# Kernel optimization log

Measured on AMD Instinct MI355X. Metric: run time of the kernel, lower is better.

Reference implementation:

```python
import jax, jax.numpy as jnp
import numpy as np
import math

NUM_LEAD = 12
PATCHES = 100  # patch_num_v * patch_num_h = 5 * 20
HEADS = 12
HID = 768
DH = HID // HEADS  # 64
SEQ = NUM_LEAD * PATCHES + NUM_LEAD + 1  # 1213
INTER = 3072
BATCH = 8


def _layer_norm(x, g, b, eps=1e-12):
    u = x.mean(-1, keepdims=True)
    s = ((x - u) ** 2).mean(-1, keepdims=True)
    return g * (x - u) / jnp.sqrt(s + eps) + b


def _lead_mask():
    # make_mask with fusion == 0: additive bias applied to query rows [0, NUM_LEAD+1)
    cols = jnp.arange(SEQ)
    # CLS row: 1 at lead-token positions 1..NUM_LEAD
    cls_row = jnp.where((cols >= 1) & (cols < NUM_LEAD + 1), 1.0, 0.0)
    # Lead rows: 1 everywhere except own patch block
    i = jnp.arange(NUM_LEAD)[:, None]
    start = NUM_LEAD + 1 + PATCHES * i
    in_block = (cols[None, :] >= start) & (cols[None, :] < start + PATCHES)
    lead_rows = jnp.where(in_block, 0.0, 1.0)
    mask = jnp.concatenate([cls_row[None, :], lead_rows], axis=0)  # [NUM_LEAD+1, SEQ]
    return mask * (-99999.0)


def setup_inputs() -> dict:
    key = jax.random.key(0)
    ks = jax.random.split(key, 12)
    std = 0.02
    d = {
        "hidden_states": jax.random.normal(ks[0], (BATCH, SEQ, HID), jnp.float32),
        "attention_mask": jnp.zeros((BATCH, 1, 1, SEQ), jnp.float32),
        "Wq": jax.random.normal(ks[1], (HID, HID), jnp.float32) * std,
        "bq": jnp.zeros((HID,), jnp.float32),
        "Wk": jax.random.normal(ks[2], (HID, HID), jnp.float32) * std,
        "bk": jnp.zeros((HID,), jnp.float32),
        "Wv": jax.random.normal(ks[3], (HID, HID), jnp.float32) * std,
        "bv": jnp.zeros((HID,), jnp.float32),
        "Wo": jax.random.normal(ks[4], (HID, HID), jnp.float32) * std,
        "bo": jnp.zeros((HID,), jnp.float32),
        "gamma1": jnp.ones((HID,), jnp.float32),
        "beta1": jnp.zeros((HID,), jnp.float32),
        "Wi": jax.random.normal(ks[5], (HID, INTER), jnp.float32) * std,
        "bi": jnp.zeros((INTER,), jnp.float32),
        "Wd": jax.random.normal(ks[6], (INTER, HID), jnp.float32) * std,
        "bd": jnp.zeros((HID,), jnp.float32),
        "gamma2": jnp.ones((HID,), jnp.float32),
        "beta2": jnp.zeros((HID,), jnp.float32),
    }
    return d


def reference(hidden_states, attention_mask, Wq, bq, Wk, bk, Wv, bv, Wo, bo,
              gamma1, beta1, Wi, bi, Wd, bd, gamma2, beta2):
    B, S, _ = hidden_states.shape

    def heads(x):  # [B,S,HID] -> [B,H,S,DH]
        return x.reshape(B, S, HEADS, DH).transpose(0, 2, 1, 3)

    q = heads(hidden_states @ Wq + bq)
    k = heads(hidden_states @ Wk + bk)
    v = heads(hidden_states @ Wv + bv)

    scores = jnp.einsum("bhqd,bhkd->bhqk", q, k) / math.sqrt(DH)
    scores = scores + attention_mask  # broadcast [B,1,1,S]
    lead_mask = _lead_mask()  # [NUM_LEAD+1, SEQ]
    scores = scores.at[:, :, : NUM_LEAD + 1, :].add(lead_mask[None, None])

    probs = jax.nn.softmax(scores, axis=-1)  # dropout is identity in eval
    ctx = jnp.einsum("bhqk,bhkd->bhqd", probs, v)
    ctx = ctx.transpose(0, 2, 1, 3).reshape(B, S, HID)

    attn_out = _layer_norm(ctx @ Wo + bo + hidden_states, gamma1, beta1)
    inter = jax.nn.gelu(attn_out @ Wi + bi, approximate=False)  # exact erf gelu
    out = _layer_norm(inter @ Wd + bd + attn_out, gamma2, beta2)
    return out
```

## Files before the change

kernel.cpp:

```cpp
#include <hip/hip_runtime.h>
#include <hip/hip_bf16.h>
#include <stdint.h>

typedef unsigned short u16;
typedef unsigned int u32;
typedef __attribute__((ext_vector_type(8))) short frag8;
typedef __attribute__((ext_vector_type(4))) float f32x4;

#define SEQ 1213
#define BATCH 8
#define HEADS 12
#define DH 64
#define HID 768
#define INTER 3072
#define BS (BATCH*SEQ)
#define LOG2E 1.44269504088896f

#define MFMA(a,b,c) __builtin_amdgcn_mfma_f32_16x16x32_bf16(a,b,c,0,0,0)

__device__ __forceinline__ float b2f(u16 u){ u32 i=((u32)u)<<16; float f; __builtin_memcpy(&f,&i,4); return f; }
__device__ __forceinline__ u16 f2b(float f){ u32 i; __builtin_memcpy(&i,&f,4); i = i + 0x7fffu + ((i>>16)&1u); return (u16)(i>>16); }
__device__ __forceinline__ u32 pack2(float a, float b){ return (u32)f2b(a) | ((u32)f2b(b)<<16); }

__device__ __forceinline__ void async16(const u16* g, u16* l){
  __builtin_amdgcn_global_load_lds((const __attribute__((address_space(1))) u32*)(uintptr_t)g,
                                   (__attribute__((address_space(3))) u32*)(uintptr_t)l, 16, 0, 0);
}

__global__ __launch_bounds__(256) void convert_arr(const void* __restrict__ src,
  u16* __restrict__ dst, int n8, const u16* __restrict__ probe)
{
  const bool f32 = (probe[0] == 0);
  int i = blockIdx.x*256 + threadIdx.x;
  if (i >= n8) return;
  u16 tmp[8];
  if (f32){
    const float* s = (const float*)src + (size_t)i*8;
#pragma unroll
    for (int j=0;j<8;j++) tmp[j] = f2b(s[j]);
  } else {
    *(uint4*)tmp = *((const uint4*)src + i);
  }
  *((uint4*)dst + i) = *(const uint4*)tmp;
}

__global__ __launch_bounds__(256) void convert_small(
  const void* bq, const void* bk, const void* bv, const void* bo,
  const void* bi, const void* bd, const void* g1, const void* be1,
  const void* g2, const void* be2, const void* am,
  u16* __restrict__ dst, const u16* __restrict__ probe)
{
  const int starts[12] = {0,768,1536,2304,3072,6144,6912,7680,8448,9216,9984,19688};
  const void* srcs[11] = {bq,bk,bv,bo,bi,bd,g1,be1,g2,be2,am};
  const bool f32 = (probe[0] == 0);
  int e = (blockIdx.x*256 + threadIdx.x) * 8;
  if (e >= 19688) return;
  int seg = 0;
#pragma unroll
  for (int k=1;k<11;k++) if (starts[k] <= e) seg = k;
  int off = e - starts[seg];
  const void* s = srcs[seg];
  u16 tmp[8];
  if (f32){
    const float* sf = (const float*)s + off;
#pragma unroll
    for (int j=0;j<8;j++) tmp[j] = f2b(sf[j]);
  } else {
    const u16* sh = (const u16*)s + off;
#pragma unroll
    for (int j=0;j<8;j++) tmp[j] = sh[j];
  }
  *(uint4*)(dst + e) = *(const uint4*)tmp;
}

__global__ __launch_bounds__(256) void transpose2(const void* __restrict__ in,
  u16* __restrict__ out, int R, int C, const u16* __restrict__ probe)
{
  const bool f32 = (probe[0] == 0);
  __shared__ u16 tile[32][33];
  const int bx = blockIdx.x*32, by = blockIdx.y*32;
  const int tx = threadIdx.x & 31, ty = threadIdx.x >> 5;
  if (f32){
    const float* inf_ = (const float*)in;
#pragma unroll
    for (int i=ty;i<32;i+=8) tile[i][tx] = f2b(inf_[(size_t)(by+i)*C + bx+tx]);
  } else {
    const u16* inh = (const u16*)in;
#pragma unroll
    for (int i=ty;i<32;i+=8) tile[i][tx] = inh[(size_t)(by+i)*C + bx+tx];
  }
  __syncthreads();
#pragma unroll
  for (int i=ty;i<32;i+=8) out[(size_t)(bx+i)*R + by+tx] = tile[tx][i];
}

__device__ __forceinline__ void gemm_tile(
    const u16* __restrict__ A, const u16* __restrict__ BT,
    int M, int K, int m0, int n0,
    u16* ldsA, u16* ldsB, f32x4 acc[4][4])
{
  const int t = threadIdx.x;
  const int w = t >> 6, l = t & 63;
  const int lw = l & 15, lh = l >> 4;
  const int rowo = (w >> 1) << 6;
  const int colo = (w & 1) << 6;
  const int srow = w*8 + (l>>3);
  const int scol = ((l&7) ^ ((l>>3)&7)) * 8;

  const u16* gpA[4]; const u16* gpB[4];
  u16* lpA[4]; u16* lpB[4];
#pragma unroll
  for (int p=0;p<4;p++){
    int ra = m0 + p*32 + srow; if (ra >= M) ra = M-1;
    gpA[p] = A  + (size_t)ra*K + scol;
    gpB[p] = BT + (size_t)(n0 + p*32 + srow)*K + scol;
    lpA[p] = ldsA + (p*32 + w*8)*64 + l*8;
    lpB[p] = ldsB + (p*32 + w*8)*64 + l*8;
  }

  const int slot0 = lw & 7;
  for (int k0 = 0; k0 < K; k0 += 64) {
    __syncthreads();
#pragma unroll
    for (int p=0;p<4;p++) async16(gpA[p] + k0, lpA[p]);
#pragma unroll
    for (int p=0;p<4;p++) async16(gpB[p] + k0, lpB[p]);
    __syncthreads();
#pragma unroll
    for (int kk=0;kk<2;kk++){
      const int slot = ((kk*4 + lh) ^ slot0) * 8;
      frag8 af[4], bf[4];
#pragma unroll
      for (int mi=0;mi<4;mi++) af[mi] = *(const frag8*)(ldsA + (rowo + mi*16 + lw)*64 + slot);
#pragma unroll
      for (int ni=0;ni<4;ni++) bf[ni] = *(const frag8*)(ldsB + (colo + ni*16 + lw)*64 + slot);
#pragma unroll
      for (int mi=0;mi<4;mi++)
#pragma unroll
        for (int ni=0;ni<4;ni++)
          acc[mi][ni] = MFMA(af[mi], bf[ni], acc[mi][ni]);
    }
  }
}

__global__ __launch_bounds__(256,2) void gemm_qkv(
  const u16* __restrict__ A, const u16* __restrict__ BT,
  const u16* __restrict__ bq, const u16* __restrict__ bk, const u16* __restrict__ bv,
  u16* __restrict__ Qo, u16* __restrict__ Ko, u16* __restrict__ Vo)
{
  __shared__ __align__(16) u16 ldsA[128*64];
  __shared__ __align__(16) u16 ldsB[128*64];
  f32x4 acc[4][4];
#pragma unroll
  for (int i=0;i<4;i++)
#pragma unroll
    for (int j=0;j<4;j++) acc[i][j] = 0.f;
  const int m0 = blockIdx.x*128, n0 = blockIdx.y*128;
  gemm_tile(A, BT, BS, HID, m0, n0, ldsA, ldsB, acc);
  const int t=threadIdx.x, w=t>>6, l=t&63, lw=l&15, lh=l>>4;
  const int rowb = m0 + ((w>>1)<<6), colb = n0 + ((w&1)<<6);
#pragma unroll
  for (int ni=0;ni<4;ni++){
    int cc = colb + ni*16 + lw;
    int which = cc / HID;
    int n2 = cc - which*HID;
    int h = n2 >> 6, d = n2 & 63;
    const u16* bp = which==0 ? bq : (which==1 ? bk : bv);
    u16* op = which==0 ? Qo : (which==1 ? Ko : Vo);
    float bias = b2f(bp[n2]);
    float scale = which==0 ? 0.125f : 1.0f;
#pragma unroll
    for (int mi=0;mi<4;mi++){
#pragma unroll
      for (int r=0;r<4;r++){
        int rr = rowb + mi*16 + lh*4 + r;
        if (rr < BS){
          int bi_ = rr / SEQ;
          int si  = rr - bi_*SEQ;
          float v = (acc[mi][ni][r] + bias) * scale;
          op[(((size_t)(bi_*HEADS + h))*SEQ + si)*64 + d] = f2b(v);
        }
      }
    }
  }
}

__global__ __launch_bounds__(256,2) void gemm_resid(
  const u16* __restrict__ A, const u16* __restrict__ BT,
  const u16* __restrict__ bias, const u16* __restrict__ resid,
  u16* __restrict__ out, int N, int K)
{
  __shared__ __align__(16) u16 ldsA[128*64];
  __shared__ __align__(16) u16 ldsB[128*64];
  f32x4 acc[4][4];
#pragma unroll
  for (int i=0;i<4;i++)
#pragma unroll
    for (int j=0;j<4;j++) acc[i][j] = 0.f;
  const int m0 = blockIdx.x*128, n0 = blockIdx.y*128;
  gemm_tile(A, BT, BS, K, m0, n0, ldsA, ldsB, acc);
  const int t=threadIdx.x, w=t>>6, l=t&63, lw=l&15, lh=l>>4;
  const int rowb = m0 + ((w>>1)<<6), colb = n0 + ((w&1)<<6);
#pragma unroll
  for (int ni=0;ni<4;ni++){
    int cc = colb + ni*16 + lw;
    float bv_ = b2f(bias[cc]);
#pragma unroll
    for (int mi=0;mi<4;mi++){
#pragma unroll
      for (int r=0;r<4;r++){
        int rr = rowb + mi*16 + lh*4 + r;
        if (rr < BS){
          float v = acc[mi][ni][r] + bv_ + b2f(resid[(size_t)rr*N + cc]);
          out[(size_t)rr*N + cc] = f2b(v);
        }
      }
    }
  }
}

__global__ __launch_bounds__(256,2) void gemm_gelu(
  const u16* __restrict__ A, const u16* __restrict__ BT,
  const u16* __restrict__ bias, u16* __restrict__ out, int N, int K)
{
  __shared__ __align__(16) u16 ldsA[128*64];
  __shared__ __align__(16) u16 ldsB[128*64];
  f32x4 acc[4][4];
#pragma unroll
  for (int i=0;i<4;i++)
#pragma unroll
    for (int j=0;j<4;j++) acc[i][j] = 0.f;
  const int m0 = blockIdx.x*128, n0 = blockIdx.y*128;
  gemm_tile(A, BT, BS, K, m0, n0, ldsA, ldsB, acc);
  const int t=threadIdx.x, w=t>>6, l=t&63, lw=l&15, lh=l>>4;
  const int rowb = m0 + ((w>>1)<<6), colb = n0 + ((w&1)<<6);
#pragma unroll
  for (int ni=0;ni<4;ni++){
    int cc = colb + ni*16 + lw;
    float bv_ = b2f(bias[cc]);
#pragma unroll
    for (int mi=0;mi<4;mi++){
#pragma unroll
      for (int r=0;r<4;r++){
        int rr = rowb + mi*16 + lh*4 + r;
        if (rr < BS){
          float v = acc[mi][ni][r] + bv_;
          v = 0.5f * v * (1.0f + erff(v * 0.70710678118654752f));
          out[(size_t)rr*N + cc] = f2b(v);
        }
      }
    }
  }
}

__global__ __launch_bounds__(512,1) void attn_kernel(
  const u16* __restrict__ Qb, const u16* __restrict__ Kb, const u16* __restrict__ Vb,
  const u16* __restrict__ amask, u16* __restrict__ ctx)
{
  __shared__ __align__(16) u16 sQP[128*72];
  __shared__ __align__(16) u16 sK[64*72];
  __shared__ __align__(16) u16 sV[64*72];
  __shared__ float sEm[64];
  const int t = threadIdx.x, w = t>>6, l = t&63, lw = l&15, lh = l>>4;
  const int bh = blockIdx.y, b = bh / HEADS;
  const int q0 = blockIdx.x * 128;
  const int h = bh % HEADS;
  const size_t hb = (size_t)bh * SEQ * 64;
  const u16* Qp = Qb + hb;
  const u16* Kp = Kb + hb;
  const u16* Vp = Vb + hb;

  {
    int r = t >> 3, c = t & 7;
#pragma unroll
    for (int i=0;i<2;i++){
      int rr = i*64 + r;
      int s = q0 + rr; if (s > SEQ-1) s = SEQ-1;
      *(uint4*)(sQP + rr*72 + c*8) = *(const uint4*)(Qp + (size_t)s*64 + c*8);
    }
  }
  __syncthreads();
  frag8 qa[2];
#pragma unroll
  for (int kk=0;kk<2;kk++) qa[kk] = *(const frag8*)(sQP + (w*16 + lw)*72 + kk*32 + lh*8);
  u16* pw = sQP + w*16*72;

  float l_p = 0.f;
  f32x4 o[4];
#pragma unroll
  for (int i=0;i<4;i++) o[i] = 0.f;
  const bool leadwave = (q0 == 0) && (w == 0);

  const int rr = t >> 3, c = t & 7;
  const int scol = (((rr>>3) ^ (c&3))<<3) + (rr&7);

  uint4 kreg, vreg; float emreg = 0.f;
  {
    int s = rr; if (s > SEQ-1) s = SEQ-1;
    kreg = *(const uint4*)(Kp + (size_t)s*64 + c*8);
    vreg = *(const uint4*)(Vp + (size_t)s*64 + c*8);
    if (t < 64) emreg = b2f(amask[b*SEQ + t]) * LOG2E;
  }

  const int nkt = (SEQ + 63) / 64;
  for (int kt = 0; kt < nkt; kt++) {
    __syncthreads();
    {
      *(uint4*)(sK + rr*72 + c*8) = kreg;
      const u16* vp = (const u16*)&vreg;
#pragma unroll
      for (int j=0;j<8;j++)
        sV[(c*8 + j)*72 + scol] = vp[j];
      if (t < 64) sEm[t] = emreg;
    }
    __syncthreads();
    if (kt+1 < nkt){
      int s = (kt+1)*64 + rr; if (s > SEQ-1) s = SEQ-1;
      kreg = *(const uint4*)(Kp + (size_t)s*64 + c*8);
      vreg = *(const uint4*)(Vp + (size_t)s*64 + c*8);
      if (t < 64){
        int sg = (kt+1)*64 + t;
        emreg = (sg < SEQ) ? b2f(amask[b*SEQ + sg]) * LOG2E : -1e30f;
      }
    }

    f32x4 st[4];
#pragma unroll
    for (int si=0;si<4;si++){
      f32x4 a0 = 0.f;
#pragma unroll
      for (int kk=0;kk<2;kk++){
        frag8 kf = *(const frag8*)(sK + (si*16 + lw)*72 + kk*32 + lh*8);
        a0 = MFMA(kf, qa[kk], a0);
      }
      st[si] = a0;
    }

#pragma unroll
    for (int si=0;si<4;si++){
      f32x4 emv = *(const f32x4*)(sEm + si*16 + lh*4);
#pragma unroll
      for (int r=0;r<4;r++)
        st[si][r] = exp2f(fmaf(st[si][r], LOG2E, emv[r]));
    }
    if (leadwave){
#pragma unroll
      for (int si=0;si<4;si++){
#pragma unroll
        for (int r=0;r<4;r++){
          int sg = kt*64 + si*16 + lh*4 + r;
          int q = lw;
          float p = st[si][r];
          if (q == 0){
            if (sg >= 1 && sg < 13) p = 0.f;
          } else if (q < 13){
            int stt = 13 + 100*(q-1);
            if (!(sg >= stt && sg < stt+100)) p = 0.f;
          }
          st[si][r] = p;
        }
      }
    }
#pragma unroll
    for (int si=0;si<4;si++)
#pragma unroll
      for (int r=0;r<4;r++) l_p += st[si][r];

#pragma unroll
    for (int si=0;si<4;si++){
      *(u32*)(pw + lw*72 + si*16 + lh*4)     = pack2(st[si][0], st[si][1]);
      *(u32*)(pw + lw*72 + si*16 + lh*4 + 2) = pack2(st[si][2], st[si][3]);
    }
    __threadfence_block();

#pragma unroll
    for (int kk=0;kk<2;kk++){
      frag8 pf = *(const frag8*)(pw + lw*72 + kk*32 + lh*8);
#pragma unroll
      for (int ni=0;ni<4;ni++){
        int d = ni*16 + lw;
        int grp = (kk*4 + lh) ^ ((d>>3) & 3);
        frag8 vf = *(const frag8*)(sV + d*72 + (grp<<3));
        o[ni] = MFMA(pf, vf, o[ni]);
      }
    }
  }

  l_p += __shfl_xor(l_p, 16);
  l_p += __shfl_xor(l_p, 32);

#pragma unroll
  for (int r=0;r<4;r++){
    float lf = __shfl(l_p, (l & 48) + ((l >> 4) << 2) + r);
    int qg = q0 + w*16 + lh*4 + r;
    if (qg < SEQ){
      float inv = 1.0f / lf;
#pragma unroll
      for (int ni=0;ni<4;ni++){
        ctx[((size_t)(b*SEQ) + qg)*HID + h*64 + ni*16 + lw] = f2b(o[ni][r] * inv);
      }
    }
  }
}

__global__ __launch_bounds__(256) void ln_kernel(const u16* __restrict__ y,
  const u16* __restrict__ g, const u16* __restrict__ be,
  u16* __restrict__ outb, float* __restrict__ outf)
{
  const int row = blockIdx.x, t = threadIdx.x;
  const u16* yp = y + (size_t)row*HID;
  float x0 = b2f(yp[t]), x1 = b2f(yp[t+256]), x2 = b2f(yp[t+512]);
  float s = x0 + x1 + x2;
  __shared__ float red[4];
#pragma unroll
  for (int off=1; off<64; off<<=1) s += __shfl_xor(s, off);
  if ((t & 63) == 0) red[t>>6] = s;
  __syncthreads();
  float u = (red[0]+red[1]+red[2]+red[3]) * (1.0f/768.0f);
  float d0=x0-u, d1=x1-u, d2=x2-u;
  float s2 = d0*d0 + d1*d1 + d2*d2;
  __syncthreads();
#pragma unroll
  for (int off=1; off<64; off<<=1) s2 += __shfl_xor(s2, off);
  if ((t & 63) == 0) red[t>>6] = s2;
  __syncthreads();
  float var = (red[0]+red[1]+red[2]+red[3]) * (1.0f/768.0f);
  float rstd = rsqrtf(var + 1e-12f);
  float v0 = b2f(g[t])    *(d0*rstd) + b2f(be[t]);
  float v1 = b2f(g[t+256])*(d1*rstd) + b2f(be[t+256]);
  float v2 = b2f(g[t+512])*(d2*rstd) + b2f(be[t+512]);
  if (outf){
    float* op = outf + (size_t)row*HID;
    op[t] = v0; op[t+256] = v1; op[t+512] = v2;
  } else {
    u16* op = outb + (size_t)row*HID;
    op[t] = f2b(v0); op[t+256] = f2b(v1); op[t+512] = f2b(v2);
  }
}

extern "C" void kernel_launch(void* const* d_in, const int* in_sizes, int n_in,
                              void* d_out, int out_size, void* d_ws, size_t ws_size,
                              hipStream_t stream)
{
  const void* hidden = d_in[0];
  const void* amask  = d_in[1];
  const void* Wq = d_in[2];  const void* bq = d_in[3];
  const void* Wk = d_in[4];  const void* bk = d_in[5];
  const void* Wv = d_in[6];  const void* bv = d_in[7];
  const void* Wo = d_in[8];  const void* bo = d_in[9];
  const void* g1 = d_in[10]; const void* be1= d_in[11];
  const void* Wi = d_in[12]; const void* bi = d_in[13];
  const void* Wd = d_in[14]; const void* bd = d_in[15];
  const void* g2 = d_in[16]; const void* be2= d_in[17];
  const u16* probe = (const u16*)g1;

  char* ws = (char*)d_ws;
  size_t off = 0;
  auto alloc = [&](size_t elems)->u16* {
    u16* p = (u16*)(ws + off);
    off += ((elems*2 + 255) & ~(size_t)255);
    return p;
  };
  u16* hiddenC = alloc((size_t)BS*HID);
  u16* smallC  = alloc((size_t)19688);
  u16* WqkvT = alloc((size_t)2304*768);
  u16* WoT   = alloc((size_t)768*768);
  u16* WiT   = alloc((size_t)3072*768);
  u16* WdT   = alloc((size_t)768*3072);
  u16* Qb    = alloc((size_t)BS*HID);
  u16* Kb    = alloc((size_t)BS*HID);
  u16* Vb    = alloc((size_t)BS*HID);
  u16* y1    = alloc((size_t)BS*HID);
  u16* interb = Qb;
  u16* ctxb  = alloc((size_t)BS*HID);
  u16* attn_out = alloc((size_t)BS*HID);
  u16* y2 = ctxb;

  const u16* c_bq = smallC;        const u16* c_bk = smallC+768;
  const u16* c_bv = smallC+1536;   const u16* c_bo = smallC+2304;
  const u16* c_bi = smallC+3072;   const u16* c_bd = smallC+6144;
  const u16* c_g1 = smallC+6912;   const u16* c_be1= smallC+7680;
  const u16* c_g2 = smallC+8448;   const u16* c_be2= smallC+9216;
  const u16* c_am = smallC+9984;

  dim3 blk(256);
  convert_arr<<<dim3((BS*HID/8 + 255)/256), blk, 0, stream>>>(hidden, hiddenC, BS*HID/8, probe);
  convert_small<<<dim3(10), blk, 0, stream>>>(bq,bk,bv,bo,bi,bd,g1,be1,g2,be2,amask, smallC, probe);
  transpose2<<<dim3(24,24),blk,0,stream>>>(Wq, WqkvT,              768, 768, probe);
  transpose2<<<dim3(24,24),blk,0,stream>>>(Wk, WqkvT + 768*768,    768, 768, probe);
  transpose2<<<dim3(24,24),blk,0,stream>>>(Wv, WqkvT + 2*768*768,  768, 768, probe);
  transpose2<<<dim3(24,24),blk,0,stream>>>(Wo, WoT, 768, 768, probe);
  transpose2<<<dim3(96,24),blk,0,stream>>>(Wi, WiT, 768, 3072, probe);
  transpose2<<<dim3(24,96),blk,0,stream>>>(Wd, WdT, 3072, 768, probe);

  gemm_qkv<<<dim3(76,18),blk,0,stream>>>(hiddenC, WqkvT, c_bq,c_bk,c_bv, Qb,Kb,Vb);
  attn_kernel<<<dim3(10,96),dim3(512),0,stream>>>(Qb,Kb,Vb, c_am, ctxb);
  gemm_resid<<<dim3(76,6),blk,0,stream>>>(ctxb, WoT, c_bo, hiddenC, y1, 768, 768);
  ln_kernel<<<dim3(BS),blk,0,stream>>>(y1, c_g1, c_be1, attn_out, nullptr);
  gemm_gelu<<<dim3(76,24),blk,0,stream>>>(attn_out, WiT, c_bi, interb, 3072, 768);
  gemm_resid<<<dim3(76,6),blk,0,stream>>>(interb, WdT, c_bd, attn_out, y2, 768, 3072);
  ln_kernel<<<dim3(BS),blk,0,stream>>>(y2, c_g2, c_be2, nullptr, (float*)d_out);
}
```

Measured before the change: 496.9 us.

## Store V transposed, double-buffer K/V tiles, keep P in registers via permlane swaps

The QKV GEMM now writes V transposed into a padded [bh][d][SEQP] layout, so the attention kernel can load V tiles with vector stores into a swizzled LDS buffer instead of scattering them element by element. K/V/mask tiles are double-buffered, which removes one barrier per key tile. The probability matrix is converted with v_cvt_pk_bf16_f32 and rearranged into MFMA operand layout with permlane swaps, avoiding the LDS round trip. In exchange, the transposed V stores from the GEMM epilogue are strided and uncoalesced, a small padding kernel is added, and LDS use grows.

```diff
diff --git a/kernel.cpp b/kernel.cpp
--- a/kernel.cpp
+++ b/kernel.cpp
@@ -8,6 +8,7 @@
 typedef __attribute__((ext_vector_type(4))) float f32x4;
 
 #define SEQ 1213
+#define SEQP 1216
 #define BATCH 8
 #define HEADS 12
 #define DH 64
@@ -20,7 +21,6 @@
 
 __device__ __forceinline__ float b2f(u16 u){ u32 i=((u32)u)<<16; float f; __builtin_memcpy(&f,&i,4); return f; }
 __device__ __forceinline__ u16 f2b(float f){ u32 i; __builtin_memcpy(&i,&f,4); i = i + 0x7fffu + ((i>>16)&1u); return (u16)(i>>16); }
-__device__ __forceinline__ u32 pack2(float a, float b){ return (u32)f2b(a) | ((u32)f2b(b)<<16); }
 
 __device__ __forceinline__ void async16(const u16* g, u16* l){
   __builtin_amdgcn_global_load_lds((const __attribute__((address_space(1))) u32*)(uintptr_t)g,
@@ -92,6 +92,15 @@
   __syncthreads();
 #pragma unroll
   for (int i=ty;i<32;i+=8) out[(size_t)(bx+i)*R + by+tx] = tile[tx][i];
+}
+
+__global__ __launch_bounds__(256) void vpad(u16* __restrict__ VT)
+{
+  int i = blockIdx.x*256 + threadIdx.x;
+  if (i < BATCH*HEADS*64*3){
+    int row = i / 3, cc = i - 3*(i/3);
+    VT[(size_t)row*SEQP + SEQ + cc] = 0;
+  }
 }
 
 __device__ __forceinline__ void gemm_tile(
@@ -146,7 +155,7 @@
 __global__ __launch_bounds__(256,2) void gemm_qkv(
   const u16* __restrict__ A, const u16* __restrict__ BT,
   const u16* __restrict__ bq, const u16* __restrict__ bk, const u16* __restrict__ bv,
-  u16* __restrict__ Qo, u16* __restrict__ Ko, u16* __restrict__ Vo)
+  u16* __restrict__ Qo, u16* __restrict__ Ko, u16* __restrict__ VT)
 {
   __shared__ __align__(16) u16 ldsA[128*64];
   __shared__ __align__(16) u16 ldsB[128*64];
@@ -166,7 +175,6 @@
     int n2 = cc - which*HID;
     int h = n2 >> 6, d = n2 & 63;
     const u16* bp = which==0 ? bq : (which==1 ? bk : bv);
-    u16* op = which==0 ? Qo : (which==1 ? Ko : Vo);
     float bias = b2f(bp[n2]);
     float scale = which==0 ? 0.125f : 1.0f;
 #pragma unroll
@@ -178,7 +186,12 @@
           int bi_ = rr / SEQ;
           int si  = rr - bi_*SEQ;
           float v = (acc[mi][ni][r] + bias) * scale;
-          op[(((size_t)(bi_*HEADS + h))*SEQ + si)*64 + d] = f2b(v);
+          if (which == 2){
+            VT[((size_t)((bi_*HEADS + h)*64 + d))*SEQP + si] = f2b(v);
+          } else {
+            u16* op = which==0 ? Qo : Ko;
+            op[(((size_t)(bi_*HEADS + h))*SEQ + si)*64 + d] = f2b(v);
+          }
         }
       }
     }
@@ -254,36 +267,50 @@
 }
 
 __global__ __launch_bounds__(512,1) void attn_kernel(
-  const u16* __restrict__ Qb, const u16* __restrict__ Kb, const u16* __restrict__ Vb,
+  const u16* __restrict__ Qb, const u16* __restrict__ Kb, const u16* __restrict__ Vt,
   const u16* __restrict__ amask, u16* __restrict__ ctx)
 {
   __shared__ __align__(16) u16 sQP[128*72];
-  __shared__ __align__(16) u16 sK[64*72];
-  __shared__ __align__(16) u16 sV[64*72];
-  __shared__ float sEm[64];
+  __shared__ __align__(16) u16 sK[2][64*72];
+  __shared__ __align__(16) u16 sV[2][64*64];
+  __shared__ float sEm[2][64];
   const int t = threadIdx.x, w = t>>6, l = t&63, lw = l&15, lh = l>>4;
   const int bh = blockIdx.y, b = bh / HEADS;
   const int q0 = blockIdx.x * 128;
-  const int h = bh % HEADS;
   const size_t hb = (size_t)bh * SEQ * 64;
   const u16* Qp = Qb + hb;
   const u16* Kp = Kb + hb;
-  const u16* Vp = Vb + hb;
+  const u16* Vp = Vt + (size_t)bh * 64 * SEQP;
+
+  const int rr = t >> 3, c = t & 7;
+  const int wsw = ((c ^ (rr&7))<<3);
+  const int cc0 = (lw&7) ^ lh;
 
   {
-    int r = t >> 3, c = t & 7;
 #pragma unroll
     for (int i=0;i<2;i++){
-      int rr = i*64 + r;
-      int s = q0 + rr; if (s > SEQ-1) s = SEQ-1;
-      *(uint4*)(sQP + rr*72 + c*8) = *(const uint4*)(Qp + (size_t)s*64 + c*8);
-    }
+      int qr = i*64 + rr;
+      int s = q0 + qr; if (s > SEQ-1) s = SEQ-1;
+      *(uint4*)(sQP + qr*72 + c*8) = *(const uint4*)(Qp + (size_t)s*64 + c*8);
+    }
+  }
+
+  uint4 kreg, vreg; float emreg = 0.f;
+  {
+    kreg = *(const uint4*)(Kp + (size_t)rr*64 + c*8);
+    vreg = *(const uint4*)(Vp + (size_t)rr*SEQP + c*8);
+    if (t < 64) emreg = b2f(amask[b*SEQ + t]) * LOG2E;
   }
   __syncthreads();
+
   frag8 qa[2];
 #pragma unroll
   for (int kk=0;kk<2;kk++) qa[kk] = *(const frag8*)(sQP + (w*16 + lw)*72 + kk*32 + lh*8);
-  u16* pw = sQP + w*16*72;
+
+  *(uint4*)(&sK[0][rr*72 + c*8]) = kreg;
+  *(uint4*)(&sV[0][rr*64 + wsw]) = vreg;
+  if (t < 64) sEm[0][t] = emreg;
+  __syncthreads();
 
   float l_p = 0.f;
   f32x4 o[4];
@@ -291,33 +318,17 @@
   for (int i=0;i<4;i++) o[i] = 0.f;
   const bool leadwave = (q0 == 0) && (w == 0);
 
-  const int rr = t >> 3, c = t & 7;
-  const int scol = (((rr>>3) ^ (c&3))<<3) + (rr&7);
-
-  uint4 kreg, vreg; float emreg = 0.f;
-  {
-    int s = rr; if (s > SEQ-1) s = SEQ-1;
-    kreg = *(const uint4*)(Kp + (size_t)s*64 + c*8);
-    vreg = *(const uint4*)(Vp + (size_t)s*64 + c*8);
-    if (t < 64) emreg = b2f(amask[b*SEQ + t]) * LOG2E;
-  }
-
   const int nkt = (SEQ + 63) / 64;
   for (int kt = 0; kt < nkt; kt++) {
-    __syncthreads();
-    {
-      *(uint4*)(sK + rr*72 + c*8) = kreg;
-      const u16* vp = (const u16*)&vreg;
-#pragma unroll
-      for (int j=0;j<8;j++)
-        sV[(c*8 + j)*72 + scol] = vp[j];
-      if (t < 64) sEm[t] = emreg;
-    }
-    __syncthreads();
-    if (kt+1 < nkt){
+    const int p = kt & 1;
+    const u16* sKp = sK[p];
+    const u16* sVp = sV[p];
+    const float* sEp = sEm[p];
+    const bool pf_next = (kt+1 < nkt);
+    if (pf_next){
       int s = (kt+1)*64 + rr; if (s > SEQ-1) s = SEQ-1;
       kreg = *(const uint4*)(Kp + (size_t)s*64 + c*8);
-      vreg = *(const uint4*)(Vp + (size_t)s*64 + c*8);
+      vreg = *(const uint4*)(Vp + (size_t)rr*SEQP + (kt+1)*64 + c*8);
       if (t < 64){
         int sg = (kt+1)*64 + t;
         emreg = (sg < SEQ) ? b2f(amask[b*SEQ + sg]) * LOG2E : -1e30f;
@@ -330,7 +341,7 @@
       f32x4 a0 = 0.f;
 #pragma unroll
       for (int kk=0;kk<2;kk++){
-        frag8 kf = *(const frag8*)(sK + (si*16 + lw)*72 + kk*32 + lh*8);
+        frag8 kf = *(const frag8*)(sKp + (si*16 + lw)*72 + kk*32 + lh*8);
         a0 = MFMA(kf, qa[kk], a0);
       }
       st[si] = a0;
@@ -338,7 +349,7 @@
 
 #pragma unroll
     for (int si=0;si<4;si++){
-      f32x4 emv = *(const f32x4*)(sEm + si*16 + lh*4);
+      f32x4 emv = *(const f32x4*)(sEp + si*16 + lh*4);
 #pragma unroll
       for (int r=0;r<4;r++)
         st[si][r] = exp2f(fmaf(st[si][r], LOG2E, emv[r]));
@@ -350,14 +361,14 @@
         for (int r=0;r<4;r++){
           int sg = kt*64 + si*16 + lh*4 + r;
           int q = lw;
-          float p = st[si][r];
+          float pv = st[si][r];
           if (q == 0){
-            if (sg >= 1 && sg < 13) p = 0.f;
+            if (sg >= 1 && sg < 13) pv = 0.f;
           } else if (q < 13){
             int stt = 13 + 100*(q-1);
-            if (!(sg >= stt && sg < stt+100)) p = 0.f;
+            if (!(sg >= stt && sg < stt+100)) pv = 0.f;
           }
-          st[si][r] = p;
+          st[si][r] = pv;
         }
       }
     }
@@ -366,29 +377,47 @@
 #pragma unroll
       for (int r=0;r<4;r++) l_p += st[si][r];
 
+    u32 pa[4], pb[4];
 #pragma unroll
     for (int si=0;si<4;si++){
-      *(u32*)(pw + lw*72 + si*16 + lh*4)     = pack2(st[si][0], st[si][1]);
-      *(u32*)(pw + lw*72 + si*16 + lh*4 + 2) = pack2(st[si][2], st[si][3]);
-    }
-    __threadfence_block();
+      asm("v_cvt_pk_bf16_f32 %0, %1, %2" : "=v"(pa[si]) : "v"(st[si][0]), "v"(st[si][1]));
+      asm("v_cvt_pk_bf16_f32 %0, %1, %2" : "=v"(pb[si]) : "v"(st[si][2]), "v"(st[si][3]));
+    }
+    asm("v_permlane32_swap_b32 %0, %1" : "+v"(pa[0]), "+v"(pa[1]));
+    asm("v_permlane32_swap_b32 %0, %1" : "+v"(pa[2]), "+v"(pa[3]));
+    asm("v_permlane32_swap_b32 %0, %1" : "+v"(pb[0]), "+v"(pb[1]));
+    asm("v_permlane32_swap_b32 %0, %1" : "+v"(pb[2]), "+v"(pb[3]));
+    asm("v_permlane16_swap_b32 %0, %1" : "+v"(pa[0]), "+v"(pa[1]));
+    asm("v_permlane16_swap_b32 %0, %1" : "+v"(pa[2]), "+v"(pa[3]));
+    asm("v_permlane16_swap_b32 %0, %1" : "+v"(pb[0]), "+v"(pb[1]));
+    asm("v_permlane16_swap_b32 %0, %1" : "+v"(pb[2]), "+v"(pb[3]));
 
 #pragma unroll
     for (int kk=0;kk<2;kk++){
-      frag8 pf = *(const frag8*)(pw + lw*72 + kk*32 + lh*8);
+      union { u32 u[4]; frag8 f; } pfu;
+      pfu.u[0] = pa[kk*2+0]; pfu.u[1] = pb[kk*2+0];
+      pfu.u[2] = pa[kk*2+1]; pfu.u[3] = pb[kk*2+1];
+      frag8 pf = pfu.f;
 #pragma unroll
       for (int ni=0;ni<4;ni++){
-        int d = ni*16 + lw;
-        int grp = (kk*4 + lh) ^ ((d>>3) & 3);
-        frag8 vf = *(const frag8*)(sV + d*72 + (grp<<3));
+        frag8 vf = *(const frag8*)(sVp + (ni*16+lw)*64 + ((cc0 ^ (kk<<2))<<3));
         o[ni] = MFMA(pf, vf, o[ni]);
       }
+    }
+
+    if (pf_next){
+      const int pn = p ^ 1;
+      *(uint4*)(&sK[pn][rr*72 + c*8]) = kreg;
+      *(uint4*)(&sV[pn][rr*64 + wsw]) = vreg;
+      if (t < 64) sEm[pn][t] = emreg;
+      __syncthreads();
     }
   }
 
   l_p += __shfl_xor(l_p, 16);
   l_p += __shfl_xor(l_p, 32);
 
+  const int h = bh % HEADS;
 #pragma unroll
   for (int r=0;r<4;r++){
     float lf = __shfl(l_p, (l & 48) + ((l >> 4) << 2) + r);
@@ -469,7 +498,7 @@
   u16* WdT   = alloc((size_t)768*3072);
   u16* Qb    = alloc((size_t)BS*HID);
   u16* Kb    = alloc((size_t)BS*HID);
-  u16* Vb    = alloc((size_t)BS*HID);
+  u16* VTb   = alloc((size_t)BS*HID);
   u16* y1    = alloc((size_t)BS*HID);
   u16* interb = Qb;
   u16* ctxb  = alloc((size_t)BS*HID);
@@ -492,9 +521,10 @@
   transpose2<<<dim3(24,24),blk,0,stream>>>(Wo, WoT, 768, 768, probe);
   transpose2<<<dim3(96,24),blk,0,stream>>>(Wi, WiT, 768, 3072, probe);
   transpose2<<<dim3(24,96),blk,0,stream>>>(Wd, WdT, 3072, 768, probe);
-
-  gemm_qkv<<<dim3(76,18),blk,0,stream>>>(hiddenC, WqkvT, c_bq,c_bk,c_bv, Qb,Kb,Vb);
-  attn_kernel<<<dim3(10,96),dim3(512),0,stream>>>(Qb,Kb,Vb, c_am, ctxb);
+  vpad<<<dim3((BATCH*HEADS*64*3 + 255)/256), blk, 0, stream>>>(VTb);
+
+  gemm_qkv<<<dim3(76,18),blk,0,stream>>>(hiddenC, WqkvT, c_bq,c_bk,c_bv, Qb,Kb,VTb);
+  attn_kernel<<<dim3(10,96),dim3(512),0,stream>>>(Qb,Kb,VTb, c_am, ctxb);
   gemm_resid<<<dim3(76,6),blk,0,stream>>>(ctxb, WoT, c_bo, hiddenC, y1, 768, 768);
   ln_kernel<<<dim3(BS),blk,0,stream>>>(y1, c_g1, c_be1, attn_out, nullptr);
   gemm_gelu<<<dim3(76,24),blk,0,stream>>>(attn_out, WiT, c_bi, interb, 3072, 768);
```

Result: slower. 524.7 us (+5.6%).
